# Optimization experiments

Hardware: AMD Instinct MI355X
Metric: run time of the kernel (lower is better)

The kernel has to match this reference:

```python
import jax, jax.numpy as jnp
import numpy as np

EPS = 1e-8
ANGULAR_WEIGHT = 0.1
L2_REG = 1e-4


def gram_schmidt_batch(A):
    # A: (B, 3, 3); orthogonalize the COLUMNS
    u1 = A[:, :, 0]
    e1 = u1 / (jnp.linalg.norm(u1, axis=1, keepdims=True) + EPS)
    a2 = A[:, :, 1]
    u2 = a2 - jnp.sum(e1 * a2, axis=1, keepdims=True) * e1
    e2 = u2 / (jnp.linalg.norm(u2, axis=1, keepdims=True) + EPS)
    a3 = A[:, :, 2]
    u3 = a3 - jnp.sum(e1 * a3, axis=1, keepdims=True) * e1 - jnp.sum(e2 * a3, axis=1, keepdims=True) * e2
    e3 = u3 / (jnp.linalg.norm(u3, axis=1, keepdims=True) + EPS)
    Q = jnp.stack([e1, e2, e3], axis=2)  # (B,3,3), columns e1,e2,e3
    det = jnp.linalg.det(Q)
    # flip third column where det < 0 to ensure proper rotation
    e3_fixed = jnp.where(det[:, None] < 0, -Q[:, :, 2], Q[:, :, 2])
    return Q.at[:, :, 2].set(e3_fixed)


def nine_d_to_rotmat(nine_d):
    A = jnp.clip(nine_d, -10.0, 10.0).reshape(-1, 3, 3)
    return gram_schmidt_batch(A)


def angular_distance(pred_9d, target_9d):
    pred_rot = nine_d_to_rotmat(pred_9d)
    target_rot = nine_d_to_rotmat(target_9d)
    # trace(pred^T @ target) = sum over all entries of elementwise product
    traces = jnp.einsum('bij,bij->b', pred_rot, target_rot)
    traces = jnp.clip(traces, -3.0 + 1e-6, 3.0 - 1e-6)
    cos_angle = jnp.clip((traces - 1.0) / 2.0, -1.0 + 1e-7, 1.0 - 1e-7)
    angles_deg = jnp.arccos(cos_angle) * (180.0 / np.pi)
    return jnp.where(jnp.isnan(angles_deg), 180.0, angles_deg)


def orthogonality_loss(nine_d):
    B = nine_d.shape[0]
    M = nine_d.reshape(B, 3, 3)
    AtA = jnp.einsum('bki,bkj->bij', M, M)
    diff = AtA - jnp.eye(3, dtype=nine_d.dtype)
    return jnp.mean(jnp.sum(diff * diff, axis=(1, 2)))


def setup_inputs() -> dict:
    key = jax.random.key(0)
    k1, k2 = jax.random.split(key)
    B = 4194304
    return {
        'pred_delta_9d': jax.random.normal(k1, (B, 9), dtype=jnp.float32),
        'target_delta_9d': jax.random.normal(k2, (B, 9), dtype=jnp.float32),
    }


def reference(pred_delta_9d, target_delta_9d):
    pred_delta_9d = jnp.clip(pred_delta_9d, -10.0, 10.0)
    pred_rot = nine_d_to_rotmat(pred_delta_9d)
    target_rot = nine_d_to_rotmat(target_delta_9d)
    diff = pred_rot - target_rot
    chordal_loss = jnp.mean(jnp.sum(diff * diff, axis=(1, 2)))
    angular_loss_term = jnp.mean(angular_distance(pred_delta_9d, target_delta_9d))
    ortho_loss = orthogonality_loss(pred_delta_9d)
    l2_loss = jnp.mean(pred_delta_9d ** 2)
    total_loss = chordal_loss + ANGULAR_WEIGHT * angular_loss_term + 0.01 * ortho_loss + L2_REG * l2_loss
    # NaN fallback: MSE between pred and target
    fallback = jnp.mean((pred_delta_9d - target_delta_9d) ** 2)
    return jnp.where(jnp.isnan(total_loss), fallback, total_loss)
```

## Files before the change

### kernel.cpp

```cpp
#include <hip/hip_runtime.h>
#include <math.h>

#define EPS_GS 1e-8f
#define RAD2DEG 57.29577951308232f
#define PI_F 3.14159265358979f

__device__ __forceinline__ float clip10(float x) {
    x = x < -10.f ? -10.f : x;
    x = x >  10.f ?  10.f : x;
    return x;
}

__device__ __forceinline__ float fsqrt(float x) { return __builtin_amdgcn_sqrtf(x); }
__device__ __forceinline__ float frcp(float x)  { return __builtin_amdgcn_rcpf(x); }

__device__ __forceinline__ float fast_acos(float x) {
    float ax = fabsf(x);
    float p = fmaf(ax, -0.0187293f, 0.0742610f);
    p = fmaf(ax, p, -0.2121144f);
    p = fmaf(ax, p, 1.5707288f);
    float pos = fsqrt(1.f - ax) * p;
    return x >= 0.f ? pos : PI_F - pos;
}

__device__ __forceinline__ void gs_rotmat(const float* v, float* R) {
    float c0x = v[0], c0y = v[3], c0z = v[6];
    float c1x = v[1], c1y = v[4], c1z = v[7];
    float c2x = v[2], c2y = v[5], c2z = v[8];

    float s1 = fmaf(c0x, c0x, fmaf(c0y, c0y, c0z*c0z));
    float inv1 = frcp(fsqrt(s1) + EPS_GS);
    float e1x = c0x*inv1, e1y = c0y*inv1, e1z = c0z*inv1;

    float d = fmaf(e1x, c1x, fmaf(e1y, c1y, e1z*c1z));
    float u2x = fmaf(-d, e1x, c1x), u2y = fmaf(-d, e1y, c1y), u2z = fmaf(-d, e1z, c1z);
    float s2 = fmaf(u2x, u2x, fmaf(u2y, u2y, u2z*u2z));
    float inv2 = frcp(fsqrt(s2) + EPS_GS);
    float e2x = u2x*inv2, e2y = u2y*inv2, e2z = u2z*inv2;

    float d1 = fmaf(e1x, c2x, fmaf(e1y, c2y, e1z*c2z));
    float d2 = fmaf(e2x, c2x, fmaf(e2y, c2y, e2z*c2z));
    float u3x = fmaf(-d1, e1x, fmaf(-d2, e2x, c2x));
    float u3y = fmaf(-d1, e1y, fmaf(-d2, e2y, c2y));
    float u3z = fmaf(-d1, e1z, fmaf(-d2, e2z, c2z));
    float s3 = fmaf(u3x, u3x, fmaf(u3y, u3y, u3z*u3z));
    float inv3 = frcp(fsqrt(s3) + EPS_GS);
    float e3x = u3x*inv3, e3y = u3y*inv3, e3z = u3z*inv3;

    float cxx = e2y*e3z - e2z*e3y;
    float cxy = e2z*e3x - e2x*e3z;
    float cxz = e2x*e3y - e2y*e3x;
    float det = fmaf(e1x, cxx, fmaf(e1y, cxy, e1z*cxz));
    if (det < 0.f) { e3x = -e3x; e3y = -e3y; e3z = -e3z; }

    R[0] = e1x; R[1] = e2x; R[2] = e3x;
    R[3] = e1y; R[4] = e2y; R[5] = e3y;
    R[6] = e1z; R[7] = e2z; R[8] = e3z;
}

__device__ __forceinline__ void accum_rot(const float* pr, const float* tg,
                                          float& lt, float& lf) {
    float pc[9], tc[9];
    #pragma unroll
    for (int m = 0; m < 9; ++m) { pc[m] = clip10(pr[m]); tc[m] = clip10(tg[m]); }

    float Rp[9], Rt[9];
    gs_rotmat(pc, Rp);
    gs_rotmat(tc, Rt);

    float chord = 0.f, tr = 0.f;
    #pragma unroll
    for (int m = 0; m < 9; ++m) {
        float d = Rp[m] - Rt[m];
        chord = fmaf(d, d, chord);
        tr    = fmaf(Rp[m], Rt[m], tr);
    }

    const float trLo = -3.0f + 1e-6f, trHi = 3.0f - 1e-6f;
    tr = tr < trLo ? trLo : (tr > trHi ? trHi : tr);
    float ca = (tr - 1.f) * 0.5f;
    const float cLo = -1.0f + 1e-7f, cHi = 1.0f - 1e-7f;
    ca = ca < cLo ? cLo : (ca > cHi ? cHi : ca);
    float ang = fast_acos(ca) * RAD2DEG;
    if (ang != ang) ang = 180.f;

    float o = 0.f;
    #pragma unroll
    for (int i = 0; i < 3; ++i) {
        #pragma unroll
        for (int j = 0; j < 3; ++j) {
            float s = fmaf(pc[i], pc[j], fmaf(pc[3+i], pc[3+j], pc[6+i]*pc[6+j]));
            s -= (i == j) ? 1.f : 0.f;
            o = fmaf(s, s, o);
        }
    }

    float l2 = 0.f, fb = 0.f;
    #pragma unroll
    for (int m = 0; m < 9; ++m) {
        l2 = fmaf(pc[m], pc[m], l2);
        float d = pc[m] - tg[m];
        fb = fmaf(d, d, fb);
    }

    lt += fmaf(0.1f, ang, chord) + fmaf(0.01f, o, (1e-4f/9.f)*l2);
    lf += fb;
}

__global__ __launch_bounds__(256)
void rot_loss_kernel(const float* __restrict__ pred, const float* __restrict__ targ,
                     double* __restrict__ acc, int B) {
    const int g    = blockIdx.x * blockDim.x + threadIdx.x;
    const int base = g * 4;

    float lt = 0.f, lf = 0.f;

    if (base + 3 < B) {
        const float4* p4 = reinterpret_cast<const float4*>(pred) + (size_t)g * 9;
        const float4* t4 = reinterpret_cast<const float4*>(targ) + (size_t)g * 9;
        float4 pv[9], tv[9];
        #pragma unroll
        for (int j = 0; j < 9; ++j) pv[j] = p4[j];
        #pragma unroll
        for (int j = 0; j < 9; ++j) tv[j] = t4[j];
        float a[36], b[36];
        #pragma unroll
        for (int j = 0; j < 9; ++j) {
            a[4*j+0] = pv[j].x; a[4*j+1] = pv[j].y; a[4*j+2] = pv[j].z; a[4*j+3] = pv[j].w;
            b[4*j+0] = tv[j].x; b[4*j+1] = tv[j].y; b[4*j+2] = tv[j].z; b[4*j+3] = tv[j].w;
        }
        #pragma unroll
        for (int k = 0; k < 4; ++k) accum_rot(&a[9*k], &b[9*k], lt, lf);
    } else if (base < B) {
        for (int r = base; r < B; ++r) {
            float a1[9], b1[9];
            for (int m = 0; m < 9; ++m) { a1[m] = pred[(size_t)r*9 + m]; b1[m] = targ[(size_t)r*9 + m]; }
            accum_rot(a1, b1, lt, lf);
        }
    }

    #pragma unroll
    for (int off = 32; off > 0; off >>= 1) {
        lt += __shfl_down(lt, off, 64);
        lf += __shfl_down(lf, off, 64);
    }
    __shared__ float st[4], sf[4];
    const int lane = threadIdx.x & 63;
    const int wid  = threadIdx.x >> 6;
    if (lane == 0) { st[wid] = lt; sf[wid] = lf; }
    __syncthreads();
    if (threadIdx.x == 0) {
        float bt = st[0] + st[1] + st[2] + st[3];
        float bf = sf[0] + sf[1] + sf[2] + sf[3];
        unsafeAtomicAdd(&acc[0], (double)bt);
        unsafeAtomicAdd(&acc[1], (double)bf);
    }
}

__global__ void finalize_kernel(const double* __restrict__ acc,
                                float* __restrict__ out, int B) {
    if (threadIdx.x == 0 && blockIdx.x == 0) {
        double total = acc[0] / (double)B;
        double fb    = acc[1] / (9.0 * (double)B);
        out[0] = isnan(total) ? (float)fb : (float)total;
    }
}

extern "C" void kernel_launch(void* const* d_in, const int* in_sizes, int n_in,
                              void* d_out, int out_size, void* d_ws, size_t ws_size,
                              hipStream_t stream) {
    const float* pred = (const float*)d_in[0];
    const float* targ = (const float*)d_in[1];
    const int n = in_sizes[0];
    const int B = n / 9;

    double* acc = (double*)d_ws;
    hipMemsetAsync(d_ws, 0, 2 * sizeof(double), stream);

    const int ngroups = (B + 3) / 4;
    const int threads = 256;
    const int blocks  = (ngroups + threads - 1) / threads;
    rot_loss_kernel<<<blocks, threads, 0, stream>>>(pred, targ, acc, B);
    finalize_kernel<<<1, 64, 0, stream>>>(acc, (float*)d_out, B);
}
```

Measured before the change: 332.3 us.

## Stage inputs through LDS with direct global-to-LDS async loads

Replaces the per-thread float4 register loads, where each thread read 36 contiguous floats, with block-wide coalesced global_load_lds transfers that place 512 rotations per block into shared memory. Each thread then computes two rotations from LDS. A separate tail kernel handles leftover rows. The aim is fully coalesced global access and lower register pressure, at the cost of 36 KB of LDS per block, which limits occupancy, and possible LDS bank conflicts from the stride-9 reads.

```diff
diff --git a/kernel.cpp b/kernel.cpp
--- a/kernel.cpp
+++ b/kernel.cpp
@@ -4,6 +4,7 @@
 #define EPS_GS 1e-8f
 #define RAD2DEG 57.29577951308232f
 #define PI_F 3.14159265358979f
+#define ROT_PER_BLOCK 512
 
 __device__ __forceinline__ float clip10(float x) {
     x = x < -10.f ? -10.f : x;
@@ -107,38 +108,7 @@
     lf += fb;
 }
 
-__global__ __launch_bounds__(256)
-void rot_loss_kernel(const float* __restrict__ pred, const float* __restrict__ targ,
-                     double* __restrict__ acc, int B) {
-    const int g    = blockIdx.x * blockDim.x + threadIdx.x;
-    const int base = g * 4;
-
-    float lt = 0.f, lf = 0.f;
-
-    if (base + 3 < B) {
-        const float4* p4 = reinterpret_cast<const float4*>(pred) + (size_t)g * 9;
-        const float4* t4 = reinterpret_cast<const float4*>(targ) + (size_t)g * 9;
-        float4 pv[9], tv[9];
-        #pragma unroll
-        for (int j = 0; j < 9; ++j) pv[j] = p4[j];
-        #pragma unroll
-        for (int j = 0; j < 9; ++j) tv[j] = t4[j];
-        float a[36], b[36];
-        #pragma unroll
-        for (int j = 0; j < 9; ++j) {
-            a[4*j+0] = pv[j].x; a[4*j+1] = pv[j].y; a[4*j+2] = pv[j].z; a[4*j+3] = pv[j].w;
-            b[4*j+0] = tv[j].x; b[4*j+1] = tv[j].y; b[4*j+2] = tv[j].z; b[4*j+3] = tv[j].w;
-        }
-        #pragma unroll
-        for (int k = 0; k < 4; ++k) accum_rot(&a[9*k], &b[9*k], lt, lf);
-    } else if (base < B) {
-        for (int r = base; r < B; ++r) {
-            float a1[9], b1[9];
-            for (int m = 0; m < 9; ++m) { a1[m] = pred[(size_t)r*9 + m]; b1[m] = targ[(size_t)r*9 + m]; }
-            accum_rot(a1, b1, lt, lf);
-        }
-    }
-
+__device__ __forceinline__ void block_reduce_atomic(float lt, float lf, double* acc) {
     #pragma unroll
     for (int off = 32; off > 0; off >>= 1) {
         lt += __shfl_down(lt, off, 64);
@@ -150,11 +120,62 @@
     if (lane == 0) { st[wid] = lt; sf[wid] = lf; }
     __syncthreads();
     if (threadIdx.x == 0) {
-        float bt = st[0] + st[1] + st[2] + st[3];
-        float bf = sf[0] + sf[1] + sf[2] + sf[3];
+        int nw = (blockDim.x + 63) >> 6;
+        float bt = 0.f, bf = 0.f;
+        for (int w = 0; w < nw; ++w) { bt += st[w]; bf += sf[w]; }
         unsafeAtomicAdd(&acc[0], (double)bt);
         unsafeAtomicAdd(&acc[1], (double)bf);
     }
+}
+
+__global__ __launch_bounds__(256)
+void rot_loss_lds(const float* __restrict__ pred, const float* __restrict__ targ,
+                  double* __restrict__ acc) {
+    __shared__ float sP[ROT_PER_BLOCK * 9];
+    __shared__ float sT[ROT_PER_BLOCK * 9];
+
+    const int tid  = threadIdx.x;
+    const int wave = tid >> 6;
+    const int lane = tid & 63;
+    const size_t chunkByte = (size_t)blockIdx.x * (ROT_PER_BLOCK * 36);
+
+    const char* gp = (const char*)pred + chunkByte;
+    const char* gt = (const char*)targ + chunkByte;
+
+    #pragma unroll
+    for (int j = wave; j < 18; j += 4) {
+        __builtin_amdgcn_global_load_lds(
+            (const __attribute__((address_space(1))) unsigned int*)(gp + j*1024 + lane*16),
+            (__attribute__((address_space(3))) unsigned int*)((char*)sP + j*1024),
+            16, 0, 0);
+    }
+    #pragma unroll
+    for (int j = wave; j < 18; j += 4) {
+        __builtin_amdgcn_global_load_lds(
+            (const __attribute__((address_space(1))) unsigned int*)(gt + j*1024 + lane*16),
+            (__attribute__((address_space(3))) unsigned int*)((char*)sT + j*1024),
+            16, 0, 0);
+    }
+    __syncthreads();
+
+    float lt = 0.f, lf = 0.f;
+    accum_rot(&sP[tid * 9],         &sT[tid * 9],         lt, lf);
+    accum_rot(&sP[(tid + 256) * 9], &sT[(tid + 256) * 9], lt, lf);
+
+    block_reduce_atomic(lt, lf, acc);
+}
+
+__global__ __launch_bounds__(256)
+void rot_loss_tail(const float* __restrict__ pred, const float* __restrict__ targ,
+                   double* __restrict__ acc, int start, int B) {
+    int r = start + blockIdx.x * blockDim.x + threadIdx.x;
+    float lt = 0.f, lf = 0.f;
+    if (r < B) {
+        float a[9], b[9];
+        for (int m = 0; m < 9; ++m) { a[m] = pred[(size_t)r*9 + m]; b[m] = targ[(size_t)r*9 + m]; }
+        accum_rot(a, b, lt, lf);
+    }
+    block_reduce_atomic(lt, lf, acc);
 }
 
 __global__ void finalize_kernel(const double* __restrict__ acc,
@@ -177,9 +198,12 @@
     double* acc = (double*)d_ws;
     hipMemsetAsync(d_ws, 0, 2 * sizeof(double), stream);
 
-    const int ngroups = (B + 3) / 4;
-    const int threads = 256;
-    const int blocks  = (ngroups + threads - 1) / threads;
-    rot_loss_kernel<<<blocks, threads, 0, stream>>>(pred, targ, acc, B);
+    const int fullBlocks = B / ROT_PER_BLOCK;
+    const int rem        = B - fullBlocks * ROT_PER_BLOCK;
+    if (fullBlocks > 0)
+        rot_loss_lds<<<fullBlocks, 256, 0, stream>>>(pred, targ, acc);
+    if (rem > 0)
+        rot_loss_tail<<<(rem + 255) / 256, 256, 0, stream>>>(
+            pred, targ, acc, fullBlocks * ROT_PER_BLOCK, B);
     finalize_kernel<<<1, 64, 0, stream>>>(acc, (float*)d_out, B);
 }
```

Result: slower. 415.6 us (+25.1%).

## Use grid-stride persistent blocks with per-block partials instead of global atomics

Applied to the files above, without the earlier changes.

The main kernel now runs a fixed grid of 2048 blocks in a grid-stride loop. Each block writes a float2 partial sum to workspace instead of doing double-precision atomic adds to two shared addresses. A 256-thread finalize kernel reduces the partials, which also removes the memset launch. This is meant to cut atomic contention and launch overhead from about 4096 blocks, but each thread keeps a float accumulator across more iterations, which may slightly change precision and latency hiding.

```diff
diff --git a/kernel.cpp b/kernel.cpp
--- a/kernel.cpp
+++ b/kernel.cpp
@@ -4,6 +4,8 @@
 #define EPS_GS 1e-8f
 #define RAD2DEG 57.29577951308232f
 #define PI_F 3.14159265358979f
+#define NBLOCKS 2048
+#define NTHREADS 256
 
 __device__ __forceinline__ float clip10(float x) {
     x = x < -10.f ? -10.f : x;
@@ -107,35 +109,38 @@
     lf += fb;
 }
 
-__global__ __launch_bounds__(256)
+__global__ __launch_bounds__(NTHREADS)
 void rot_loss_kernel(const float* __restrict__ pred, const float* __restrict__ targ,
-                     double* __restrict__ acc, int B) {
-    const int g    = blockIdx.x * blockDim.x + threadIdx.x;
-    const int base = g * 4;
+                     float2* __restrict__ partial, int B) {
+    const int ngroups  = (B + 3) >> 2;
+    const int nthreads = gridDim.x * blockDim.x;
 
     float lt = 0.f, lf = 0.f;
 
-    if (base + 3 < B) {
-        const float4* p4 = reinterpret_cast<const float4*>(pred) + (size_t)g * 9;
-        const float4* t4 = reinterpret_cast<const float4*>(targ) + (size_t)g * 9;
-        float4 pv[9], tv[9];
-        #pragma unroll
-        for (int j = 0; j < 9; ++j) pv[j] = p4[j];
-        #pragma unroll
-        for (int j = 0; j < 9; ++j) tv[j] = t4[j];
-        float a[36], b[36];
-        #pragma unroll
-        for (int j = 0; j < 9; ++j) {
-            a[4*j+0] = pv[j].x; a[4*j+1] = pv[j].y; a[4*j+2] = pv[j].z; a[4*j+3] = pv[j].w;
-            b[4*j+0] = tv[j].x; b[4*j+1] = tv[j].y; b[4*j+2] = tv[j].z; b[4*j+3] = tv[j].w;
-        }
-        #pragma unroll
-        for (int k = 0; k < 4; ++k) accum_rot(&a[9*k], &b[9*k], lt, lf);
-    } else if (base < B) {
-        for (int r = base; r < B; ++r) {
-            float a1[9], b1[9];
-            for (int m = 0; m < 9; ++m) { a1[m] = pred[(size_t)r*9 + m]; b1[m] = targ[(size_t)r*9 + m]; }
-            accum_rot(a1, b1, lt, lf);
+    for (int g = blockIdx.x * blockDim.x + threadIdx.x; g < ngroups; g += nthreads) {
+        const int base = g * 4;
+        if (base + 3 < B) {
+            const float4* p4 = reinterpret_cast<const float4*>(pred) + (size_t)g * 9;
+            const float4* t4 = reinterpret_cast<const float4*>(targ) + (size_t)g * 9;
+            float4 pv[9], tv[9];
+            #pragma unroll
+            for (int j = 0; j < 9; ++j) pv[j] = p4[j];
+            #pragma unroll
+            for (int j = 0; j < 9; ++j) tv[j] = t4[j];
+            float a[36], b[36];
+            #pragma unroll
+            for (int j = 0; j < 9; ++j) {
+                a[4*j+0] = pv[j].x; a[4*j+1] = pv[j].y; a[4*j+2] = pv[j].z; a[4*j+3] = pv[j].w;
+                b[4*j+0] = tv[j].x; b[4*j+1] = tv[j].y; b[4*j+2] = tv[j].z; b[4*j+3] = tv[j].w;
+            }
+            #pragma unroll
+            for (int k = 0; k < 4; ++k) accum_rot(&a[9*k], &b[9*k], lt, lf);
+        } else {
+            for (int r = base; r < B; ++r) {
+                float a1[9], b1[9];
+                for (int m = 0; m < 9; ++m) { a1[m] = pred[(size_t)r*9 + m]; b1[m] = targ[(size_t)r*9 + m]; }
+                accum_rot(a1, b1, lt, lf);
+            }
         }
     }
 
@@ -152,16 +157,32 @@
     if (threadIdx.x == 0) {
         float bt = st[0] + st[1] + st[2] + st[3];
         float bf = sf[0] + sf[1] + sf[2] + sf[3];
-        unsafeAtomicAdd(&acc[0], (double)bt);
-        unsafeAtomicAdd(&acc[1], (double)bf);
-    }
-}
-
-__global__ void finalize_kernel(const double* __restrict__ acc,
-                                float* __restrict__ out, int B) {
-    if (threadIdx.x == 0 && blockIdx.x == 0) {
-        double total = acc[0] / (double)B;
-        double fb    = acc[1] / (9.0 * (double)B);
+        partial[blockIdx.x] = make_float2(bt, bf);
+    }
+}
+
+__global__ __launch_bounds__(256)
+void finalize_kernel(const float2* __restrict__ partial, int nparts,
+                     float* __restrict__ out, int B) {
+    double t = 0.0, f = 0.0;
+    for (int i = threadIdx.x; i < nparts; i += 256) {
+        float2 p = partial[i];
+        t += (double)p.x;
+        f += (double)p.y;
+    }
+    #pragma unroll
+    for (int off = 32; off > 0; off >>= 1) {
+        t += __shfl_down(t, off, 64);
+        f += __shfl_down(f, off, 64);
+    }
+    __shared__ double st[4], sf[4];
+    const int lane = threadIdx.x & 63;
+    const int wid  = threadIdx.x >> 6;
+    if (lane == 0) { st[wid] = t; sf[wid] = f; }
+    __syncthreads();
+    if (threadIdx.x == 0) {
+        double total = (st[0] + st[1] + st[2] + st[3]) / (double)B;
+        double fb    = (sf[0] + sf[1] + sf[2] + sf[3]) / (9.0 * (double)B);
         out[0] = isnan(total) ? (float)fb : (float)total;
     }
 }
@@ -174,12 +195,8 @@
     const int n = in_sizes[0];
     const int B = n / 9;
 
-    double* acc = (double*)d_ws;
-    hipMemsetAsync(d_ws, 0, 2 * sizeof(double), stream);
-
-    const int ngroups = (B + 3) / 4;
-    const int threads = 256;
-    const int blocks  = (ngroups + threads - 1) / threads;
-    rot_loss_kernel<<<blocks, threads, 0, stream>>>(pred, targ, acc, B);
-    finalize_kernel<<<1, 64, 0, stream>>>(acc, (float*)d_out, B);
-}
+    float2* partial = (float2*)d_ws;
+
+    rot_loss_kernel<<<NBLOCKS, NTHREADS, 0, stream>>>(pred, targ, partial, B);
+    finalize_kernel<<<1, 256, 0, stream>>>(partial, NBLOCKS, (float*)d_out, B);
+}
```

Result: slower. 368.6 us (+10.9%).
